# Optimization experiments

Hardware: AMD Instinct MI355X
Metric: run time of the kernel (lower is better)

The kernel has to match this reference:

```python
import jax, jax.numpy as jnp
import numpy as np

N_NODES = 50000


def gcn_conv(x, edge_index, W, b):
    """PyG GCNConv: h = x @ W; add self-loops; symmetric deg^-1/2 norm; scatter-add; + bias."""
    h = x @ W                                   # [N, C_out]
    n = x.shape[0]
    loops = jnp.arange(n, dtype=edge_index.dtype)
    src = jnp.concatenate([edge_index[0], loops])   # [E + N]
    dst = jnp.concatenate([edge_index[1], loops])   # [E + N]
    deg = jax.ops.segment_sum(jnp.ones_like(src, dtype=h.dtype), dst, num_segments=n)
    dinv = jnp.where(deg > 0, jax.lax.rsqrt(deg), 0.0)
    norm = dinv[src] * dinv[dst]                # [E + N]
    msg = h[src] * norm[:, None]                # gather + edgewise scale
    out = jax.ops.segment_sum(msg, dst, num_segments=n)  # scatter-add
    return out + b


def setup_inputs() -> dict:
    key = jax.random.key(0)
    k1, k2, k3, k4 = jax.random.split(key, 4)
    x = jax.random.normal(k1, (N_NODES, 128), dtype=jnp.float32)
    edge_index = jax.random.randint(k2, (2, 800000), 0, N_NODES, dtype=jnp.int32)
    W1 = jax.random.normal(k3, (128, 128), dtype=jnp.float32) * (1.0 / np.sqrt(128))
    b1 = jnp.zeros((128,), dtype=jnp.float32)
    W2 = jax.random.normal(k4, (128, 64), dtype=jnp.float32) * (1.0 / np.sqrt(128))
    b2 = jnp.zeros((64,), dtype=jnp.float32)
    return {"x": x, "edge_index": edge_index, "W1": W1, "b1": b1, "W2": W2, "b2": b2}


def reference(x, edge_index, W1, b1, W2, b2):
    h = gcn_conv(x, edge_index, W1, b1)
    h = jax.nn.relu(h)
    out = gcn_conv(h, edge_index, W2, b2)
    return out
```

## Files before the change

kernel.cpp:

```cpp
#include <hip/hip_runtime.h>
#include <hip/hip_bf16.h>
#include <math.h>

#define N_NODES 50000
#define N_EDGES 800000
#define NSLICE 8
#define SLICE_NODES 6400
#define CSR_W 48
#define EDGE_CHUNKS ((N_EDGES + 1023) / 1024)
#define BUILD_BLOCKS (EDGE_CHUNKS * NSLICE)
#define GEMM1_BLOCKS ((N_NODES / 16 + 1) / 2)
#define GROUPS 196

typedef unsigned int uint;
typedef unsigned short ushort;
typedef __attribute__((ext_vector_type(8))) short bf16x8;
typedef __attribute__((ext_vector_type(4))) float f32x4;

__device__ __forceinline__ float bf16_lo(uint u) { return __uint_as_float(u << 16); }
__device__ __forceinline__ float bf16_hi(uint u) { return __uint_as_float(u & 0xFFFF0000u); }
__device__ __forceinline__ ushort f2bf(float a) {
    return __bfloat16_as_ushort(__float2bfloat16(a));
}
__device__ __forceinline__ uint pack_bf2(float a, float b) {
    return ((uint)f2bf(b) << 16) | (uint)f2bf(a);
}

__global__ __launch_bounds__(256) void setup_kernel(const float* __restrict__ W1,
                                                    const float* __restrict__ W2,
                                                    int* __restrict__ counts,
                                                    ushort* __restrict__ W1t,
                                                    ushort* __restrict__ W2t,
                                                    ushort* __restrict__ h1pad,
                                                    ushort* __restrict__ h2pad) {
    int i = blockIdx.x * 256 + threadIdx.x;
    if (i < N_NODES + 1) { counts[i] = 0; return; }
    i -= N_NODES + 1;
    if (i < 128 * 128) {
        int k = i >> 7, n = i & 127;
        W1t[n * 128 + k] = f2bf(W1[i]);
        return;
    }
    i -= 128 * 128;
    if (i < 128 * 64) {
        int k = i >> 6, n = i & 63;
        W2t[n * 128 + k] = f2bf(W2[i]);
        return;
    }
    i -= 128 * 64;
    if (i < 128) { h1pad[i] = 0; return; }
    i -= 128;
    if (i < 64) h2pad[i] = 0;
}

__global__ __launch_bounds__(256) void fused_gemm1_build(const int* __restrict__ ei,
                                                         int* __restrict__ counts,
                                                         int* __restrict__ csr,
                                                         const float* __restrict__ X,
                                                         const ushort* __restrict__ W1t,
                                                         ushort* __restrict__ H) {
    int grp = blockIdx.x / 40;
    int r = blockIdx.x % 40;
    if (r < 32) {
        int b = grp * 32 + r;
        int slice = b & (NSLICE - 1);
        int chunk = b / NSLICE;
        int lo = slice * SLICE_NODES;
        int hi = lo + SLICE_NODES;
        int base = chunk * 1024 + threadIdx.x * 4;
        if (base + 3 < N_EDGES) {
            int4 d = *reinterpret_cast<const int4*>(ei + N_EDGES + base);
            int4 s = *reinterpret_cast<const int4*>(ei + base);
            if (d.x >= lo && d.x < hi) {
                int rr = atomicAdd(&counts[d.x], 1);
                if (rr < CSR_W) csr[d.x * CSR_W + rr] = s.x;
            }
            if (d.y >= lo && d.y < hi) {
                int rr = atomicAdd(&counts[d.y], 1);
                if (rr < CSR_W) csr[d.y * CSR_W + rr] = s.y;
            }
            if (d.z >= lo && d.z < hi) {
                int rr = atomicAdd(&counts[d.z], 1);
                if (rr < CSR_W) csr[d.z * CSR_W + rr] = s.z;
            }
            if (d.w >= lo && d.w < hi) {
                int rr = atomicAdd(&counts[d.w], 1);
                if (rr < CSR_W) csr[d.w * CSR_W + rr] = s.w;
            }
        }
        return;
    }
    int bid = grp * 8 + (r - 32);
    int lane = threadIdx.x & 63;
    int w = threadIdx.x >> 6;
    int m = lane & 15;
    int q = lane >> 4;
    int rowTile = bid * 2 + (w >> 1);
    int nbase = (w & 1) * 64;
    if (rowTile >= N_NODES / 16) return;

    const float* arow = X + (size_t)(rowTile * 16 + m) * 128 + q * 8;
    bf16x8 afrag[4];
#pragma unroll
    for (int kt = 0; kt < 4; kt++) {
        float4 lo4 = *reinterpret_cast<const float4*>(arow + kt * 32);
        float4 hi4 = *reinterpret_cast<const float4*>(arow + kt * 32 + 4);
        uint4 u;
        u.x = pack_bf2(lo4.x, lo4.y);
        u.y = pack_bf2(lo4.z, lo4.w);
        u.z = pack_bf2(hi4.x, hi4.y);
        u.w = pack_bf2(hi4.z, hi4.w);
        afrag[kt] = *reinterpret_cast<bf16x8*>(&u);
    }

    const ushort* brow = W1t + (size_t)(nbase + m) * 128 + q * 8;
    f32x4 acc[4];
#pragma unroll
    for (int nt = 0; nt < 4; nt++) {
        acc[nt] = {0.f, 0.f, 0.f, 0.f};
        const ushort* bp = brow + (size_t)nt * 16 * 128;
#pragma unroll
        for (int kt = 0; kt < 4; kt++) {
            bf16x8 bfrag = *reinterpret_cast<const bf16x8*>(bp + kt * 32);
            acc[nt] = __builtin_amdgcn_mfma_f32_16x16x32_bf16(afrag[kt], bfrag, acc[nt], 0, 0, 0);
        }
    }

    int rbase = rowTile * 16 + q * 4;
#pragma unroll
    for (int rr = 0; rr < 4; rr++) {
#pragma unroll
        for (int nt = 0; nt < 4; nt++) {
            H[(size_t)(rbase + rr) * 128 + nbase + nt * 16 + m] = f2bf(acc[nt][rr]);
        }
    }
}

__global__ __launch_bounds__(256) void gemm2_kernel(const ushort* __restrict__ Ain,
                                                    const ushort* __restrict__ Wt,
                                                    const int* __restrict__ counts,
                                                    ushort* __restrict__ H) {
    int lane = threadIdx.x & 63;
    int w = threadIdx.x >> 6;
    int m = lane & 15;
    int q = lane >> 4;
    int rowTile = blockIdx.x * 4 + w;
    if (rowTile >= N_NODES / 16) return;

    const ushort* arow = Ain + (size_t)(rowTile * 16 + m) * 128 + q * 8;
    bf16x8 afrag[4];
#pragma unroll
    for (int kt = 0; kt < 4; kt++)
        afrag[kt] = *reinterpret_cast<const bf16x8*>(arow + kt * 32);

    const ushort* brow = Wt + (size_t)m * 128 + q * 8;
    f32x4 acc[4];
#pragma unroll
    for (int nt = 0; nt < 4; nt++) {
        acc[nt] = {0.f, 0.f, 0.f, 0.f};
        const ushort* bp = brow + (size_t)nt * 16 * 128;
#pragma unroll
        for (int kt = 0; kt < 4; kt++) {
            bf16x8 bfrag = *reinterpret_cast<const bf16x8*>(bp + kt * 32);
            acc[nt] = __builtin_amdgcn_mfma_f32_16x16x32_bf16(afrag[kt], bfrag, acc[nt], 0, 0, 0);
        }
    }

    int rbase = rowTile * 16 + q * 4;
#pragma unroll
    for (int r = 0; r < 4; r++) {
        float dn = rsqrtf((float)(counts[rbase + r] + 1));
#pragma unroll
        for (int nt = 0; nt < 4; nt++) {
            H[(size_t)(rbase + r) * 64 + nt * 16 + m] = f2bf(acc[nt][r] * dn);
        }
    }
}

template <int C, bool RELU, bool OUT_BF16, bool SRC_SCALE>
__global__ __launch_bounds__(256) void agg_kernel(const __hip_bfloat16* __restrict__ Hb,
                                                  const int* __restrict__ counts,
                                                  const int* __restrict__ csr,
                                                  const float* __restrict__ bias,
                                                  void* __restrict__ OUT) {
    int wave = threadIdx.x >> 6;
    int lane = threadIdx.x & 63;
    int n = blockIdx.x * 4 + wave;
    if (n >= N_NODES) return;

    int cntF = counts[n];
    float dn = rsqrtf((float)(cntF + 1));
    int cnt = (cntF < CSR_W) ? cntF : CSR_W;
    int e0 = n * CSR_W;
    int my = (lane < cnt) ? csr[e0 + lane] : N_NODES;
    float mys = 1.f;
    if constexpr (SRC_SCALE) mys = rsqrtf((float)(counts[my] + 1));

    if constexpr (C == 128) {
        int ql = lane & 15;
        int quarter = lane >> 4;
        float a[8];
        {
            uint4 u = reinterpret_cast<const uint4*>(Hb + (size_t)n * C)[ql];
            float self = SRC_SCALE ? dn : 1.f;
            a[0] = quarter ? 0.f : self * bf16_lo(u.x);
            a[1] = quarter ? 0.f : self * bf16_hi(u.x);
            a[2] = quarter ? 0.f : self * bf16_lo(u.y);
            a[3] = quarter ? 0.f : self * bf16_hi(u.y);
            a[4] = quarter ? 0.f : self * bf16_lo(u.z);
            a[5] = quarter ? 0.f : self * bf16_hi(u.z);
            a[6] = quarter ? 0.f : self * bf16_lo(u.w);
            a[7] = quarter ? 0.f : self * bf16_hi(u.w);
        }
        for (int j = 0; j < cnt; j += 32) {
            int rem = cnt - j;
            int s[8];
            float ds[8];
            uint4 v[8];
#pragma unroll
            for (int k = 0; k < 8; k++) {
                s[k] = __shfl(my, j + 4 * k + quarter, 64);
                if (SRC_SCALE) ds[k] = __shfl(mys, j + 4 * k + quarter, 64);
            }
#pragma unroll
            for (int k = 0; k < 8; k++) {
                if (4 * k < rem)
                    v[k] = reinterpret_cast<const uint4*>(Hb + (size_t)s[k] * C)[ql];
                else
                    v[k] = make_uint4(0, 0, 0, 0);
            }
#pragma unroll
            for (int k = 0; k < 8; k++) {
                float w0 = SRC_SCALE ? ds[k] : 1.f;
                a[0] = fmaf(w0, bf16_lo(v[k].x), a[0]);
                a[1] = fmaf(w0, bf16_hi(v[k].x), a[1]);
                a[2] = fmaf(w0, bf16_lo(v[k].y), a[2]);
                a[3] = fmaf(w0, bf16_hi(v[k].y), a[3]);
                a[4] = fmaf(w0, bf16_lo(v[k].z), a[4]);
                a[5] = fmaf(w0, bf16_hi(v[k].z), a[5]);
                a[6] = fmaf(w0, bf16_lo(v[k].w), a[6]);
                a[7] = fmaf(w0, bf16_hi(v[k].w), a[7]);
            }
        }
#pragma unroll
        for (int r = 0; r < 8; r++) {
            a[r] += __shfl_xor(a[r], 16, 64);
            a[r] += __shfl_xor(a[r], 32, 64);
        }
        if (quarter == 0) {
            float o[8];
#pragma unroll
            for (int r = 0; r < 8; r++) {
                o[r] = fmaf(a[r], dn, bias[8 * ql + r]);
                if (RELU) o[r] = fmaxf(o[r], 0.f);
            }
            if constexpr (OUT_BF16) {
                uint4 u;
                u.x = pack_bf2(o[0], o[1]);
                u.y = pack_bf2(o[2], o[3]);
                u.z = pack_bf2(o[4], o[5]);
                u.w = pack_bf2(o[6], o[7]);
                reinterpret_cast<uint4*>(OUT)[(size_t)n * 16 + ql] = u;
            } else {
                reinterpret_cast<float4*>(OUT)[(size_t)n * 32 + 2 * ql] =
                    make_float4(o[0], o[1], o[2], o[3]);
                reinterpret_cast<float4*>(OUT)[(size_t)n * 32 + 2 * ql + 1] =
                    make_float4(o[4], o[5], o[6], o[7]);
            }
        }
    } else {
        int gl = lane & 7;
        int group = lane >> 3;
        float a[8];
        {
            uint4 u = reinterpret_cast<const uint4*>(Hb + (size_t)n * C)[gl];
            a[0] = group ? 0.f : bf16_lo(u.x);
            a[1] = group ? 0.f : bf16_hi(u.x);
            a[2] = group ? 0.f : bf16_lo(u.y);
            a[3] = group ? 0.f : bf16_hi(u.y);
            a[4] = group ? 0.f : bf16_lo(u.z);
            a[5] = group ? 0.f : bf16_hi(u.z);
            a[6] = group ? 0.f : bf16_lo(u.w);
            a[7] = group ? 0.f : bf16_hi(u.w);
        }
        {
            int s[8];
            uint4 v[8];
#pragma unroll
            for (int k = 0; k < 8; k++) s[k] = __shfl(my, 8 * k + group, 64);
#pragma unroll
            for (int k = 0; k < 8; k++) {
                if (8 * k < cnt)
                    v[k] = reinterpret_cast<const uint4*>(Hb + (size_t)s[k] * C)[gl];
                else
                    v[k] = make_uint4(0, 0, 0, 0);
            }
#pragma unroll
            for (int k = 0; k < 8; k++) {
                a[0] += bf16_lo(v[k].x);
                a[1] += bf16_hi(v[k].x);
                a[2] += bf16_lo(v[k].y);
                a[3] += bf16_hi(v[k].y);
                a[4] += bf16_lo(v[k].z);
                a[5] += bf16_hi(v[k].z);
                a[6] += bf16_lo(v[k].w);
                a[7] += bf16_hi(v[k].w);
            }
        }
#pragma unroll
        for (int r = 0; r < 8; r++) {
            a[r] += __shfl_xor(a[r], 8, 64);
            a[r] += __shfl_xor(a[r], 16, 64);
            a[r] += __shfl_xor(a[r], 32, 64);
        }
        if (group == 0) {
            float o[8];
#pragma unroll
            for (int r = 0; r < 8; r++) {
                o[r] = fmaf(a[r], dn, bias[8 * gl + r]);
                if (RELU) o[r] = fmaxf(o[r], 0.f);
            }
            if constexpr (OUT_BF16) {
                uint4 u;
                u.x = pack_bf2(o[0], o[1]);
                u.y = pack_bf2(o[2], o[3]);
                u.z = pack_bf2(o[4], o[5]);
                u.w = pack_bf2(o[6], o[7]);
                reinterpret_cast<uint4*>(OUT)[(size_t)n * 8 + gl] = u;
            } else {
                reinterpret_cast<float4*>(OUT)[(size_t)n * 16 + 2 * gl] =
                    make_float4(o[0], o[1], o[2], o[3]);
                reinterpret_cast<float4*>(OUT)[(size_t)n * 16 + 2 * gl + 1] =
                    make_float4(o[4], o[5], o[6], o[7]);
            }
        }
    }
}

extern "C" void kernel_launch(void* const* d_in, const int* in_sizes, int n_in,
                              void* d_out, int out_size, void* d_ws, size_t ws_size,
                              hipStream_t stream) {
    const float* x  = (const float*)d_in[0];
    const int*   ei = (const int*)d_in[1];
    const float* W1 = (const float*)d_in[2];
    const float* b1 = (const float*)d_in[3];
    const float* W2 = (const float*)d_in[4];
    const float* b2 = (const float*)d_in[5];
    float* out = (float*)d_out;

    char* ws = (char*)d_ws;
    auto alloc = [&](size_t bytes) -> char* {
        char* p = ws;
        ws += (bytes + 255) / 256 * 256;
        return p;
    };
    int* counts = (int*)alloc((size_t)(N_NODES + 1) * 4);
    int* csr = (int*)alloc((size_t)N_NODES * CSR_W * 4);
    ushort* W1t = (ushort*)alloc((size_t)128 * 128 * 2);
    ushort* W2t = (ushort*)alloc((size_t)64 * 128 * 2);
    ushort* h1 = (ushort*)alloc((size_t)(N_NODES + 1) * 128 * 2);
    ushort* g1 = (ushort*)alloc((size_t)N_NODES * 128 * 2);
    ushort* h2 = (ushort*)alloc((size_t)(N_NODES + 1) * 64 * 2);

    const int SETUP_N = (N_NODES + 1) + 128 * 128 + 128 * 64 + 128 + 64;
    setup_kernel<<<(SETUP_N + 255) / 256, 256, 0, stream>>>(
        W1, W2, counts, W1t, W2t, h1 + (size_t)N_NODES * 128, h2 + (size_t)N_NODES * 64);
    fused_gemm1_build<<<GROUPS * 40, 256, 0, stream>>>(ei, counts, csr, x, W1t, h1);
    agg_kernel<128, true, true, true><<<(N_NODES + 3) / 4, 256, 0, stream>>>(
        (const __hip_bfloat16*)h1, counts, csr, b1, g1);
    gemm2_kernel<<<(N_NODES / 16 + 3) / 4, 256, 0, stream>>>(g1, W2t, counts, h2);
    agg_kernel<64, false, false, false><<<(N_NODES + 3) / 4, 256, 0, stream>>>(
        (const __hip_bfloat16*)h2, counts, csr, b2, out);
}
```

Baseline: 125.3 us.

## Fuse layer-1 aggregation with layer-2 GEMM through LDS

Merges the first aggregation kernel and the second GEMM into one kernel. Each block aggregates four nodes, stages the bf16 ReLU output in shared memory, and wave 0 then runs the MFMA against W2 and writes the scaled h2 rows. This removes the g1 intermediate buffer's global write and read plus one kernel launch. In exchange, each MFMA tile carries only 4 real rows of 16, a block-wide barrier is added, three waves sit idle during the GEMM, and W2t is re-read by every block. The generic agg_kernel template is split into specialised kernels.

```diff
diff --git a/kernel.cpp b/kernel.cpp
--- a/kernel.cpp
+++ b/kernel.cpp
@@ -8,8 +8,6 @@
 #define SLICE_NODES 6400
 #define CSR_W 48
 #define EDGE_CHUNKS ((N_EDGES + 1023) / 1024)
-#define BUILD_BLOCKS (EDGE_CHUNKS * NSLICE)
-#define GEMM1_BLOCKS ((N_NODES / 16 + 1) / 2)
 #define GROUPS 196
 
 typedef unsigned int uint;
@@ -136,53 +134,125 @@
     }
 }
 
-__global__ __launch_bounds__(256) void gemm2_kernel(const ushort* __restrict__ Ain,
-                                                    const ushort* __restrict__ Wt,
-                                                    const int* __restrict__ counts,
-                                                    ushort* __restrict__ H) {
+__global__ __launch_bounds__(256) void agg1_gemm2_kernel(
+    const __hip_bfloat16* __restrict__ Hb, const int* __restrict__ counts,
+    const int* __restrict__ csr, const float* __restrict__ bias,
+    const ushort* __restrict__ W2t, ushort* __restrict__ H2) {
+    __shared__ uint4 g1lds[4][16];
+
+    int wave = threadIdx.x >> 6;
     int lane = threadIdx.x & 63;
-    int w = threadIdx.x >> 6;
-    int m = lane & 15;
-    int q = lane >> 4;
-    int rowTile = blockIdx.x * 4 + w;
-    if (rowTile >= N_NODES / 16) return;
-
-    const ushort* arow = Ain + (size_t)(rowTile * 16 + m) * 128 + q * 8;
-    bf16x8 afrag[4];
-#pragma unroll
-    for (int kt = 0; kt < 4; kt++)
-        afrag[kt] = *reinterpret_cast<const bf16x8*>(arow + kt * 32);
-
-    const ushort* brow = Wt + (size_t)m * 128 + q * 8;
-    f32x4 acc[4];
-#pragma unroll
-    for (int nt = 0; nt < 4; nt++) {
-        acc[nt] = {0.f, 0.f, 0.f, 0.f};
-        const ushort* bp = brow + (size_t)nt * 16 * 128;
-#pragma unroll
-        for (int kt = 0; kt < 4; kt++) {
-            bf16x8 bfrag = *reinterpret_cast<const bf16x8*>(bp + kt * 32);
-            acc[nt] = __builtin_amdgcn_mfma_f32_16x16x32_bf16(afrag[kt], bfrag, acc[nt], 0, 0, 0);
-        }
-    }
-
-    int rbase = rowTile * 16 + q * 4;
-#pragma unroll
-    for (int r = 0; r < 4; r++) {
-        float dn = rsqrtf((float)(counts[rbase + r] + 1));
+    int n = blockIdx.x * 4 + wave;
+
+    int cntF = counts[n];
+    float dn = rsqrtf((float)(cntF + 1));
+    int cnt = (cntF < CSR_W) ? cntF : CSR_W;
+    int my = (lane < cnt) ? csr[n * CSR_W + lane] : N_NODES;
+    float mys = rsqrtf((float)(counts[my] + 1));
+
+    int ql = lane & 15;
+    int quarter = lane >> 4;
+    float a[8];
+    {
+        uint4 u = reinterpret_cast<const uint4*>(Hb + (size_t)n * 128)[ql];
+        float self = dn;
+        a[0] = quarter ? 0.f : self * bf16_lo(u.x);
+        a[1] = quarter ? 0.f : self * bf16_hi(u.x);
+        a[2] = quarter ? 0.f : self * bf16_lo(u.y);
+        a[3] = quarter ? 0.f : self * bf16_hi(u.y);
+        a[4] = quarter ? 0.f : self * bf16_lo(u.z);
+        a[5] = quarter ? 0.f : self * bf16_hi(u.z);
+        a[6] = quarter ? 0.f : self * bf16_lo(u.w);
+        a[7] = quarter ? 0.f : self * bf16_hi(u.w);
+    }
+    for (int j = 0; j < cnt; j += 32) {
+        int rem = cnt - j;
+        int s[8];
+        float ds[8];
+        uint4 v[8];
+#pragma unroll
+        for (int k = 0; k < 8; k++) {
+            s[k] = __shfl(my, j + 4 * k + quarter, 64);
+            ds[k] = __shfl(mys, j + 4 * k + quarter, 64);
+        }
+#pragma unroll
+        for (int k = 0; k < 8; k++) {
+            if (4 * k < rem)
+                v[k] = reinterpret_cast<const uint4*>(Hb + (size_t)s[k] * 128)[ql];
+            else
+                v[k] = make_uint4(0, 0, 0, 0);
+        }
+#pragma unroll
+        for (int k = 0; k < 8; k++) {
+            a[0] = fmaf(ds[k], bf16_lo(v[k].x), a[0]);
+            a[1] = fmaf(ds[k], bf16_hi(v[k].x), a[1]);
+            a[2] = fmaf(ds[k], bf16_lo(v[k].y), a[2]);
+            a[3] = fmaf(ds[k], bf16_hi(v[k].y), a[3]);
+            a[4] = fmaf(ds[k], bf16_lo(v[k].z), a[4]);
+            a[5] = fmaf(ds[k], bf16_hi(v[k].z), a[5]);
+            a[6] = fmaf(ds[k], bf16_lo(v[k].w), a[6]);
+            a[7] = fmaf(ds[k], bf16_hi(v[k].w), a[7]);
+        }
+    }
+#pragma unroll
+    for (int r = 0; r < 8; r++) {
+        a[r] += __shfl_xor(a[r], 16, 64);
+        a[r] += __shfl_xor(a[r], 32, 64);
+    }
+    if (quarter == 0) {
+        float o[8];
+#pragma unroll
+        for (int r = 0; r < 8; r++) {
+            o[r] = fmaxf(fmaf(a[r], dn, bias[8 * ql + r]), 0.f);
+        }
+        uint4 u;
+        u.x = pack_bf2(o[0], o[1]);
+        u.y = pack_bf2(o[2], o[3]);
+        u.z = pack_bf2(o[4], o[5]);
+        u.w = pack_bf2(o[6], o[7]);
+        g1lds[wave][ql] = u;
+    }
+    __syncthreads();
+
+    if (wave == 0) {
+        int m = lane & 15;
+        int q = lane >> 4;
+        bf16x8 afrag[4];
+#pragma unroll
+        for (int kt = 0; kt < 4; kt++)
+            afrag[kt] = *reinterpret_cast<const bf16x8*>(&g1lds[m & 3][kt * 4 + q]);
+
+        const ushort* brow = W2t + (size_t)m * 128 + q * 8;
+        f32x4 acc[4];
 #pragma unroll
         for (int nt = 0; nt < 4; nt++) {
-            H[(size_t)(rbase + r) * 64 + nt * 16 + m] = f2bf(acc[nt][r] * dn);
-        }
-    }
-}
-
-template <int C, bool RELU, bool OUT_BF16, bool SRC_SCALE>
-__global__ __launch_bounds__(256) void agg_kernel(const __hip_bfloat16* __restrict__ Hb,
-                                                  const int* __restrict__ counts,
-                                                  const int* __restrict__ csr,
-                                                  const float* __restrict__ bias,
-                                                  void* __restrict__ OUT) {
+            acc[nt] = {0.f, 0.f, 0.f, 0.f};
+            const ushort* bp = brow + (size_t)nt * 16 * 128;
+#pragma unroll
+            for (int kt = 0; kt < 4; kt++) {
+                bf16x8 bfrag = *reinterpret_cast<const bf16x8*>(bp + kt * 32);
+                acc[nt] = __builtin_amdgcn_mfma_f32_16x16x32_bf16(afrag[kt], bfrag, acc[nt], 0, 0, 0);
+            }
+        }
+        if (q == 0) {
+            int n0 = blockIdx.x * 4;
+#pragma unroll
+            for (int r = 0; r < 4; r++) {
+                float dn2 = rsqrtf((float)(counts[n0 + r] + 1));
+#pragma unroll
+                for (int nt = 0; nt < 4; nt++) {
+                    H2[(size_t)(n0 + r) * 64 + nt * 16 + m] = f2bf(acc[nt][r] * dn2);
+                }
+            }
+        }
+    }
+}
+
+__global__ __launch_bounds__(256) void agg2_kernel(const __hip_bfloat16* __restrict__ Hb,
+                                                   const int* __restrict__ counts,
+                                                   const int* __restrict__ csr,
+                                                   const float* __restrict__ bias,
+                                                   float* __restrict__ OUT) {
     int wave = threadIdx.x >> 6;
     int lane = threadIdx.x & 63;
     int n = blockIdx.x * 4 + wave;
@@ -191,149 +261,60 @@
     int cntF = counts[n];
     float dn = rsqrtf((float)(cntF + 1));
     int cnt = (cntF < CSR_W) ? cntF : CSR_W;
-    int e0 = n * CSR_W;
-    int my = (lane < cnt) ? csr[e0 + lane] : N_NODES;
-    float mys = 1.f;
-    if constexpr (SRC_SCALE) mys = rsqrtf((float)(counts[my] + 1));
-
-    if constexpr (C == 128) {
-        int ql = lane & 15;
-        int quarter = lane >> 4;
-        float a[8];
-        {
-            uint4 u = reinterpret_cast<const uint4*>(Hb + (size_t)n * C)[ql];
-            float self = SRC_SCALE ? dn : 1.f;
-            a[0] = quarter ? 0.f : self * bf16_lo(u.x);
-            a[1] = quarter ? 0.f : self * bf16_hi(u.x);
-            a[2] = quarter ? 0.f : self * bf16_lo(u.y);
-            a[3] = quarter ? 0.f : self * bf16_hi(u.y);
-            a[4] = quarter ? 0.f : self * bf16_lo(u.z);
-            a[5] = quarter ? 0.f : self * bf16_hi(u.z);
-            a[6] = quarter ? 0.f : self * bf16_lo(u.w);
-            a[7] = quarter ? 0.f : self * bf16_hi(u.w);
-        }
-        for (int j = 0; j < cnt; j += 32) {
-            int rem = cnt - j;
-            int s[8];
-            float ds[8];
-            uint4 v[8];
-#pragma unroll
-            for (int k = 0; k < 8; k++) {
-                s[k] = __shfl(my, j + 4 * k + quarter, 64);
-                if (SRC_SCALE) ds[k] = __shfl(mys, j + 4 * k + quarter, 64);
-            }
-#pragma unroll
-            for (int k = 0; k < 8; k++) {
-                if (4 * k < rem)
-                    v[k] = reinterpret_cast<const uint4*>(Hb + (size_t)s[k] * C)[ql];
-                else
-                    v[k] = make_uint4(0, 0, 0, 0);
-            }
-#pragma unroll
-            for (int k = 0; k < 8; k++) {
-                float w0 = SRC_SCALE ? ds[k] : 1.f;
-                a[0] = fmaf(w0, bf16_lo(v[k].x), a[0]);
-                a[1] = fmaf(w0, bf16_hi(v[k].x), a[1]);
-                a[2] = fmaf(w0, bf16_lo(v[k].y), a[2]);
-                a[3] = fmaf(w0, bf16_hi(v[k].y), a[3]);
-                a[4] = fmaf(w0, bf16_lo(v[k].z), a[4]);
-                a[5] = fmaf(w0, bf16_hi(v[k].z), a[5]);
-                a[6] = fmaf(w0, bf16_lo(v[k].w), a[6]);
-                a[7] = fmaf(w0, bf16_hi(v[k].w), a[7]);
-            }
-        }
-#pragma unroll
-        for (int r = 0; r < 8; r++) {
-            a[r] += __shfl_xor(a[r], 16, 64);
-            a[r] += __shfl_xor(a[r], 32, 64);
-        }
-        if (quarter == 0) {
-            float o[8];
-#pragma unroll
-            for (int r = 0; r < 8; r++) {
-                o[r] = fmaf(a[r], dn, bias[8 * ql + r]);
-                if (RELU) o[r] = fmaxf(o[r], 0.f);
-            }
-            if constexpr (OUT_BF16) {
-                uint4 u;
-                u.x = pack_bf2(o[0], o[1]);
-                u.y = pack_bf2(o[2], o[3]);
-                u.z = pack_bf2(o[4], o[5]);
-                u.w = pack_bf2(o[6], o[7]);
-                reinterpret_cast<uint4*>(OUT)[(size_t)n * 16 + ql] = u;
-            } else {
-                reinterpret_cast<float4*>(OUT)[(size_t)n * 32 + 2 * ql] =
-                    make_float4(o[0], o[1], o[2], o[3]);
-                reinterpret_cast<float4*>(OUT)[(size_t)n * 32 + 2 * ql + 1] =
-                    make_float4(o[4], o[5], o[6], o[7]);
-            }
-        }
-    } else {
-        int gl = lane & 7;
-        int group = lane >> 3;
-        float a[8];
-        {
-            uint4 u = reinterpret_cast<const uint4*>(Hb + (size_t)n * C)[gl];
-            a[0] = group ? 0.f : bf16_lo(u.x);
-            a[1] = group ? 0.f : bf16_hi(u.x);
-            a[2] = group ? 0.f : bf16_lo(u.y);
-            a[3] = group ? 0.f : bf16_hi(u.y);
-            a[4] = group ? 0.f : bf16_lo(u.z);
-            a[5] = group ? 0.f : bf16_hi(u.z);
-            a[6] = group ? 0.f : bf16_lo(u.w);
-            a[7] = group ? 0.f : bf16_hi(u.w);
-        }
-        {
-            int s[8];
-            uint4 v[8];
-#pragma unroll
-            for (int k = 0; k < 8; k++) s[k] = __shfl(my, 8 * k + group, 64);
-#pragma unroll
-            for (int k = 0; k < 8; k++) {
-                if (8 * k < cnt)
-                    v[k] = reinterpret_cast<const uint4*>(Hb + (size_t)s[k] * C)[gl];
-                else
-                    v[k] = make_uint4(0, 0, 0, 0);
-            }
-#pragma unroll
-            for (int k = 0; k < 8; k++) {
-                a[0] += bf16_lo(v[k].x);
-                a[1] += bf16_hi(v[k].x);
-                a[2] += bf16_lo(v[k].y);
-                a[3] += bf16_hi(v[k].y);
-                a[4] += bf16_lo(v[k].z);
-                a[5] += bf16_hi(v[k].z);
-                a[6] += bf16_lo(v[k].w);
-                a[7] += bf16_hi(v[k].w);
-            }
-        }
-#pragma unroll
-        for (int r = 0; r < 8; r++) {
-            a[r] += __shfl_xor(a[r], 8, 64);
-            a[r] += __shfl_xor(a[r], 16, 64);
-            a[r] += __shfl_xor(a[r], 32, 64);
-        }
-        if (group == 0) {
-            float o[8];
-#pragma unroll
-            for (int r = 0; r < 8; r++) {
-                o[r] = fmaf(a[r], dn, bias[8 * gl + r]);
-                if (RELU) o[r] = fmaxf(o[r], 0.f);
-            }
-            if constexpr (OUT_BF16) {
-                uint4 u;
-                u.x = pack_bf2(o[0], o[1]);
-                u.y = pack_bf2(o[2], o[3]);
-                u.z = pack_bf2(o[4], o[5]);
-                u.w = pack_bf2(o[6], o[7]);
-                reinterpret_cast<uint4*>(OUT)[(size_t)n * 8 + gl] = u;
-            } else {
-                reinterpret_cast<float4*>(OUT)[(size_t)n * 16 + 2 * gl] =
-                    make_float4(o[0], o[1], o[2], o[3]);
-                reinterpret_cast<float4*>(OUT)[(size_t)n * 16 + 2 * gl + 1] =
-                    make_float4(o[4], o[5], o[6], o[7]);
-            }
-        }
+    int my = (lane < cnt) ? csr[n * CSR_W + lane] : N_NODES;
+
+    int gl = lane & 7;
+    int group = lane >> 3;
+    float a[8];
+    {
+        uint4 u = reinterpret_cast<const uint4*>(Hb + (size_t)n * 64)[gl];
+        a[0] = group ? 0.f : bf16_lo(u.x);
+        a[1] = group ? 0.f : bf16_hi(u.x);
+        a[2] = group ? 0.f : bf16_lo(u.y);
+        a[3] = group ? 0.f : bf16_hi(u.y);
+        a[4] = group ? 0.f : bf16_lo(u.z);
+        a[5] = group ? 0.f : bf16_hi(u.z);
+        a[6] = group ? 0.f : bf16_lo(u.w);
+        a[7] = group ? 0.f : bf16_hi(u.w);
+    }
+    {
+        int s[8];
+        uint4 v[8];
+#pragma unroll
+        for (int k = 0; k < 8; k++) s[k] = __shfl(my, 8 * k + group, 64);
+#pragma unroll
+        for (int k = 0; k < 8; k++) {
+            if (8 * k < cnt)
+                v[k] = reinterpret_cast<const uint4*>(Hb + (size_t)s[k] * 64)[gl];
+            else
+                v[k] = make_uint4(0, 0, 0, 0);
+        }
+#pragma unroll
+        for (int k = 0; k < 8; k++) {
+            a[0] += bf16_lo(v[k].x);
+            a[1] += bf16_hi(v[k].x);
+            a[2] += bf16_lo(v[k].y);
+            a[3] += bf16_hi(v[k].y);
+            a[4] += bf16_lo(v[k].z);
+            a[5] += bf16_hi(v[k].z);
+            a[6] += bf16_lo(v[k].w);
+            a[7] += bf16_hi(v[k].w);
+        }
+    }
+#pragma unroll
+    for (int r = 0; r < 8; r++) {
+        a[r] += __shfl_xor(a[r], 8, 64);
+        a[r] += __shfl_xor(a[r], 16, 64);
+        a[r] += __shfl_xor(a[r], 32, 64);
+    }
+    if (group == 0) {
+        float o[8];
+#pragma unroll
+        for (int r = 0; r < 8; r++) o[r] = fmaf(a[r], dn, bias[8 * gl + r]);
+        reinterpret_cast<float4*>(OUT)[(size_t)n * 16 + 2 * gl] =
+            make_float4(o[0], o[1], o[2], o[3]);
+        reinterpret_cast<float4*>(OUT)[(size_t)n * 16 + 2 * gl + 1] =
+            make_float4(o[4], o[5], o[6], o[7]);
     }
 }
 
@@ -359,16 +340,14 @@
     ushort* W1t = (ushort*)alloc((size_t)128 * 128 * 2);
     ushort* W2t = (ushort*)alloc((size_t)64 * 128 * 2);
     ushort* h1 = (ushort*)alloc((size_t)(N_NODES + 1) * 128 * 2);
-    ushort* g1 = (ushort*)alloc((size_t)N_NODES * 128 * 2);
     ushort* h2 = (ushort*)alloc((size_t)(N_NODES + 1) * 64 * 2);
 
     const int SETUP_N = (N_NODES + 1) + 128 * 128 + 128 * 64 + 128 + 64;
     setup_kernel<<<(SETUP_N + 255) / 256, 256, 0, stream>>>(
         W1, W2, counts, W1t, W2t, h1 + (size_t)N_NODES * 128, h2 + (size_t)N_NODES * 64);
     fused_gemm1_build<<<GROUPS * 40, 256, 0, stream>>>(ei, counts, csr, x, W1t, h1);
-    agg_kernel<128, true, true, true><<<(N_NODES + 3) / 4, 256, 0, stream>>>(
-        (const __hip_bfloat16*)h1, counts, csr, b1, g1);
-    gemm2_kernel<<<(N_NODES / 16 + 3) / 4, 256, 0, stream>>>(g1, W2t, counts, h2);
-    agg_kernel<64, false, false, false><<<(N_NODES + 3) / 4, 256, 0, stream>>>(
+    agg1_gemm2_kernel<<<N_NODES / 4, 256, 0, stream>>>(
+        (const __hip_bfloat16*)h1, counts, csr, b1, W2t, h2);
+    agg2_kernel<<<(N_NODES + 3) / 4, 256, 0, stream>>>(
         (const __hip_bfloat16*)h2, counts, csr, b2, out);
 }
```

Measured after the change: 128.3 us. 1.02x slower.
